# Kernel optimization log

Hardware: AMD Instinct MI355X
Metric: run time of the kernel (lower is better)

Reference implementation:

```python
import jax, jax.numpy as jnp
import numpy as np
from jax import lax

BN_EPS = 1e-5


def setup_inputs() -> dict:
    key = jax.random.key(0)
    ks = jax.random.split(key, 4)
    B, C1, H, W = 16, 256, 64, 64
    E, C2, K = 4, 256, 3
    x = jax.random.normal(ks[0], (B, C1, H, W), dtype=jnp.float32)
    w_route = jax.random.normal(ks[1], (E, C1), dtype=jnp.float32) * 0.02
    b_route = jnp.zeros((E,), dtype=jnp.float32)
    w_experts = jax.random.normal(ks[2], (E, C2, C1, K, K), dtype=jnp.float32) * 0.02
    bn_gamma = jnp.ones((C2,), dtype=jnp.float32)
    bn_beta = jnp.zeros((C2,), dtype=jnp.float32)
    bn_mean = jnp.zeros((C2,), dtype=jnp.float32)
    bn_var = jnp.ones((C2,), dtype=jnp.float32)
    return {"x": x, "w_route": w_route, "b_route": b_route,
            "w_experts": w_experts, "bn_gamma": bn_gamma, "bn_beta": bn_beta,
            "bn_mean": bn_mean, "bn_var": bn_var}


def reference(x, w_route, b_route, w_experts, bn_gamma, bn_beta, bn_mean, bn_var):
    # Routing: global average pool -> linear -> sigmoid. [B, E]
    pooled = jnp.mean(x, axis=(2, 3))
    routing = jax.nn.sigmoid(pooled @ w_route.T + b_route)

    # All num_experts conv passes in one grouped-output conv (same math as the
    # per-expert loop in the original): stack expert filters along out-channels.
    E, Co, Ci, kh, kw = w_experts.shape
    w = w_experts.reshape(E * Co, Ci, kh, kw)
    pad = kh // 2  # autopad(3) = 1
    y = lax.conv_general_dilated(
        x, w, window_strides=(1, 1), padding=[(pad, pad), (pad, pad)],
        dimension_numbers=("NCHW", "OIHW", "NCHW"))  # [B, E*Co, H, W]
    B, _, Ho, Wo = y.shape
    y = y.reshape(B, E, Co, Ho, Wo)

    # Per-sample weighted sum over experts.
    out = jnp.einsum("beohw,be->bohw", y, routing)

    # BatchNorm2d (inference form: running stats) + SiLU.
    inv = bn_gamma / jnp.sqrt(bn_var + BN_EPS)
    out = out * inv[None, :, None, None] + (bn_beta - bn_mean * inv)[None, :, None, None]
    return jax.nn.silu(out)
```

## Files before the change

kernel.cpp:

```cpp
#include <hip/hip_runtime.h>
#include <stdint.h>

typedef unsigned int uint;
typedef unsigned short ushort;
typedef __attribute__((ext_vector_type(8))) short short8;
typedef __attribute__((ext_vector_type(4))) float f32x4;

__device__ float  g_pooled[16 * 256];
__device__ ushort g_wct[16 * 9 * 256 * 256];
__device__ ushort g_xt[16 * 64 * 64 * 256];
__device__ uint   g_isf32;

__device__ __forceinline__ float bf2f(ushort u) {
    return __uint_as_float(((uint)u) << 16);
}
__device__ __forceinline__ ushort f2bf(float f) {
    uint u = __float_as_uint(f);
    return (ushort)((u + 0x7fffu + ((u >> 16) & 1u)) >> 16);
}

__global__ void detect_zero_kernel(const uint* __restrict__ bn_g_u) {
    int t = threadIdx.x;
    for (int i = t; i < 16 * 256; i += 256) g_pooled[i] = 0.f;
    if (t == 0) g_isf32 = (bn_g_u[0] == 0x3F800000u) ? 1u : 0u;
}

__global__ __launch_bounds__(256) void xt_pool_kernel(const void* __restrict__ xraw) {
    __shared__ float tf[64 * 65];
    uint* tile = (uint*)tf;
    const int c0 = blockIdx.x * 64, h = blockIdx.y, b = blockIdx.z;
    const int t = threadIdx.x;
    uint* xtu = (uint*)g_xt;
    const uint isf32 = g_isf32;
    if (isf32) {
        const float* xf = (const float*)xraw;
#pragma unroll
        for (int p = 0; p < 16; ++p) {
            int idx = p * 256 + t;
            int cil = idx >> 6, w = idx & 63;
            tf[cil * 65 + w] = xf[(((size_t)(b * 256 + c0 + cil)) * 64 + h) * 64 + w];
        }
        __syncthreads();
#pragma unroll
        for (int p = 0; p < 8; ++p) {
            int w = p * 8 + (t >> 5), cid = t & 31;
            uint lo = f2bf(tf[(2 * cid) * 65 + w]);
            uint hi = f2bf(tf[(2 * cid + 1) * 65 + w]);
            xtu[(((size_t)b * 64 + h) * 64 + w) * 128 + (c0 >> 1) + cid] = lo | (hi << 16);
        }
        if (t < 64) {
            float s = 0.f;
#pragma unroll
            for (int w = 0; w < 64; ++w) s += tf[t * 65 + w];
            atomicAdd(&g_pooled[b * 256 + c0 + t], s);
        }
    } else {
        const uint* xu = (const uint*)xraw;
#pragma unroll
        for (int p = 0; p < 8; ++p) {
            int cil = p * 8 + (t >> 5), wd = t & 31;
            tile[cil * 33 + wd] =
                xu[(((size_t)(b * 256 + c0 + cil)) * 64 + h) * 32 + wd];
        }
        __syncthreads();
#pragma unroll
        for (int p = 0; p < 8; ++p) {
            int w = p * 8 + (t >> 5), cid = t & 31;
            uint a = tile[(2 * cid) * 33 + (w >> 1)];
            uint bb = tile[(2 * cid + 1) * 33 + (w >> 1)];
            uint lo = (w & 1) ? (a >> 16) : (a & 0xffffu);
            uint hi = (w & 1) ? (bb >> 16) : (bb & 0xffffu);
            xtu[(((size_t)b * 64 + h) * 64 + w) * 128 + (c0 >> 1) + cid] = lo | (hi << 16);
        }
        if (t < 64) {
            float s = 0.f;
#pragma unroll
            for (int wd = 0; wd < 32; ++wd) {
                uint u = tile[t * 33 + wd];
                s += __uint_as_float(u << 16) + __uint_as_float(u & 0xffff0000u);
            }
            atomicAdd(&g_pooled[b * 256 + c0 + t], s);
        }
    }
}

__global__ __launch_bounds__(256) void wcomb_kernel(const void* __restrict__ w_exp,
                                                    const void* __restrict__ w_route,
                                                    const void* __restrict__ b_route) {
    __shared__ float s_rout[64];
    const int co = blockIdx.x, ci = threadIdx.x;
    const uint isf32 = g_isf32;
    if (ci < 64) {
        int b = ci >> 2, e = ci & 3;
        float s;
        if (isf32) {
            const float* wr = (const float*)w_route;
            s = ((const float*)b_route)[e];
            for (int c = 0; c < 256; ++c)
                s += g_pooled[b * 256 + c] * (1.f / 4096.f) * wr[e * 256 + c];
        } else {
            const ushort* wr = (const ushort*)w_route;
            s = bf2f(((const ushort*)b_route)[e]);
            for (int c = 0; c < 256; ++c)
                s += g_pooled[b * 256 + c] * (1.f / 4096.f) * bf2f(wr[e * 256 + c]);
        }
        s_rout[ci] = 1.f / (1.f + __expf(-s));
    }
    float we[4][9];
    if (isf32) {
        const float* wf = (const float*)w_exp;
#pragma unroll
        for (int e = 0; e < 4; ++e) {
            const float* p = wf + (((size_t)e * 256 + co) * 256 + ci) * 9;
#pragma unroll
            for (int tp = 0; tp < 9; ++tp) we[e][tp] = p[tp];
        }
    } else {
        const ushort* wb = (const ushort*)w_exp;
#pragma unroll
        for (int e = 0; e < 4; ++e) {
            const ushort* p = wb + (((size_t)e * 256 + co) * 256 + ci) * 9;
#pragma unroll
            for (int tp = 0; tp < 9; ++tp) we[e][tp] = bf2f(p[tp]);
        }
    }
    __syncthreads();
    for (int b = 0; b < 16; ++b) {
        float r0 = s_rout[b * 4 + 0], r1 = s_rout[b * 4 + 1];
        float r2 = s_rout[b * 4 + 2], r3 = s_rout[b * 4 + 3];
#pragma unroll
        for (int tp = 0; tp < 9; ++tp) {
            float a = r0 * we[0][tp] + r1 * we[1][tp] + r2 * we[2][tp] + r3 * we[3][tp];
            g_wct[(((size_t)b * 9 + tp) * 256 + co) * 256 + ci] = f2bf(a);
        }
    }
}

__device__ __forceinline__ void load_iter(int it, int t, int h0,
                                          const ushort* __restrict__ wct_p,
                                          const ushort* __restrict__ xt_p,
                                          short8 wv[6], short8 xv[2]) {
    const int cc = it / 3, kh = it - cc * 3;
    const int ci0 = cc * 32;
#pragma unroll
    for (int i = 0; i < 6; ++i) {
        int f = i * 4096 + t * 16;
        int kw = f >> 13;
        int rem = f & 8191;
        int col = rem >> 6;
        int cio = (rem & 63) >> 1;
        wv[i] = *(const short8*)(wct_p +
            (((size_t)(kh * 3 + kw) * 256 + col) * 256 + ci0 + cio));
    }
#pragma unroll
    for (int i = 0; i < 2; ++i) {
        int f = i * 4096 + t * 16;
        int r = f >> 12;
        int rem = f & 4095;
        int col = rem >> 6;
        int cio = (rem & 63) >> 1;
        int h_in = h0 + kh - 1 + r;
        if (h_in >= 0 && h_in < 64)
            xv[i] = *(const short8*)(xt_p + (((size_t)h_in * 64 + col) * 256 + ci0 + cio));
        else
            xv[i] = (short8){0, 0, 0, 0, 0, 0, 0, 0};
    }
}

__global__ __launch_bounds__(256) void conv_kernel(
    const void* __restrict__ bn_g, const void* __restrict__ bn_b,
    const void* __restrict__ bn_m, const void* __restrict__ bn_v,
    void* __restrict__ outv) {
    __shared__ __align__(16) ushort s_x[2 * 66 * 32];
    __shared__ __align__(16) ushort s_w[3 * 128 * 32];
    __shared__ float bn_inv[128], bn_add[128];

    const int t = threadIdx.x;
    const int lane = t & 63;
    const int q = lane >> 4, l16 = lane & 15;
    const int wave = __builtin_amdgcn_readfirstlane(t >> 6);
    const int u = blockIdx.x;
    const int pair = u & 31, hw = u >> 5;
    const int b = pair >> 1;
    const int co0 = (pair & 1) * 128;
    const int h0 = hw * 2;
    const int wm = wave & 1, wn = wave >> 1;
    const uint isf32 = g_isf32;

    if (t < 128) {
        int co = co0 + t;
        float g, be, mn, vr;
        if (isf32) {
            g = ((const float*)bn_g)[co]; be = ((const float*)bn_b)[co];
            mn = ((const float*)bn_m)[co]; vr = ((const float*)bn_v)[co];
        } else {
            g = bf2f(((const ushort*)bn_g)[co]); be = bf2f(((const ushort*)bn_b)[co]);
            mn = bf2f(((const ushort*)bn_m)[co]); vr = bf2f(((const ushort*)bn_v)[co]);
        }
        float inv = g * __frsqrt_rn(vr + 1e-5f);
        bn_inv[t] = inv;
        bn_add[t] = be - mn * inv;
        int r = t >> 6, side = (t >> 5) & 1, ci = t & 31;
        s_x[(r * 66 + side * 65) * 32 + ci] = 0;
    }

    f32x4 acc[4][4];
#pragma unroll
    for (int mt = 0; mt < 4; ++mt)
#pragma unroll
        for (int nt = 0; nt < 4; ++nt) acc[mt][nt] = (f32x4){0.f, 0.f, 0.f, 0.f};

    const ushort* xt_p  = g_xt  + (size_t)b * 64 * 64 * 256;
    const ushort* wct_p = g_wct + (size_t)b * 9 * 256 * 256 + (size_t)co0 * 256;

    short8 wv[6], xv[2];
    load_iter(0, t, h0, wct_p, xt_p, wv, xv);

    for (int it = 0; it < 24; ++it) {
        __syncthreads();
#pragma unroll
        for (int i = 0; i < 6; ++i)
            *(short8*)((char*)s_w + i * 4096 + t * 16) = wv[i];
#pragma unroll
        for (int i = 0; i < 2; ++i) {
            int f = i * 4096 + t * 16;
            int r = f >> 12;
            int rem = f & 4095;
            *(short8*)((char*)s_x + r * 4224 + 64 + rem) = xv[i];
        }
        __syncthreads();
        short8 wv2[6], xv2[2];
        int itn = (it + 1 < 24) ? it + 1 : 23;
        load_iter(itn, t, h0, wct_p, xt_p, wv2, xv2);
#pragma unroll
        for (int kw = 0; kw < 3; ++kw) {
            short8 a[4], bf[4];
#pragma unroll
            for (int mt = 0; mt < 4; ++mt)
                a[mt] = *(const short8*)(s_w + ((kw * 128 + wm * 64 + mt * 16 + l16) * 32 + q * 8));
#pragma unroll
            for (int nt = 0; nt < 4; ++nt)
                bf[nt] = *(const short8*)(s_x + ((wn * 66 + nt * 16 + l16 + kw) * 32 + q * 8));
#pragma unroll
            for (int mt = 0; mt < 4; ++mt)
#pragma unroll
                for (int nt = 0; nt < 4; ++nt)
                    acc[mt][nt] = __builtin_amdgcn_mfma_f32_16x16x32_bf16(
                        a[mt], bf[nt], acc[mt][nt], 0, 0, 0);
        }
#pragma unroll
        for (int i = 0; i < 6; ++i) wv[i] = wv2[i];
        xv[0] = xv2[0]; xv[1] = xv2[1];
    }

#pragma unroll
    for (int mt = 0; mt < 4; ++mt) {
        int co_l = wm * 64 + mt * 16 + q * 4;
#pragma unroll
        for (int i = 0; i < 4; ++i) {
            float inv = bn_inv[co_l + i], add = bn_add[co_l + i];
            int co = co0 + co_l + i;
#pragma unroll
            for (int nt = 0; nt < 4; ++nt) {
                int n_local = wn * 64 + nt * 16 + l16;
                int h = h0 + (n_local >> 6), w = n_local & 63;
                float v = acc[mt][nt][i] * inv + add;
                float s = v / (1.f + __expf(-v));
                size_t idx = (((size_t)b * 256 + co) * 64 + h) * 64 + w;
                if (isf32) ((float*)outv)[idx] = s;
                else       ((ushort*)outv)[idx] = f2bf(s);
            }
        }
    }
}

extern "C" void kernel_launch(void* const* d_in, const int* in_sizes, int n_in,
                              void* d_out, int out_size, void* d_ws, size_t ws_size,
                              hipStream_t stream) {
    const void* x       = d_in[0];
    const void* w_route = d_in[1];
    const void* b_route = d_in[2];
    const void* w_exp   = d_in[3];
    const void* bn_g    = d_in[4];
    const void* bn_b    = d_in[5];
    const void* bn_m    = d_in[6];
    const void* bn_v    = d_in[7];
    (void)d_ws; (void)ws_size;

    detect_zero_kernel<<<1, 256, 0, stream>>>((const uint*)bn_g);
    xt_pool_kernel<<<dim3(4, 64, 16), 256, 0, stream>>>(x);
    wcomb_kernel<<<256, 256, 0, stream>>>(w_exp, w_route, b_route);
    conv_kernel<<<1024, 256, 0, stream>>>(bn_g, bn_b, bn_m, bn_v, d_out);
}
```

Baseline: 256.4 us.

## Vectorize transpose and weight-combine loads, pad conv LDS rows against bank conflicts

The x transpose kernel now reads float4 and writes uint4 instead of scalar elements. The weight-combine kernel stages expert weights through shared memory with coalesced float4 loads and splits the routing dot products across all threads with a reduction. The conv kernel pads its LDS rows from 32 to 40 bf16 elements so the MFMA operand reads hit fewer LDS bank conflicts, at the cost of more shared memory per block.

Result: no change. 257.2 us (+0.3%).

```diff
diff --git a/kernel.cpp b/kernel.cpp
--- a/kernel.cpp
+++ b/kernel.cpp
@@ -33,20 +33,31 @@
     uint* xtu = (uint*)g_xt;
     const uint isf32 = g_isf32;
     if (isf32) {
-        const float* xf = (const float*)xraw;
-#pragma unroll
-        for (int p = 0; p < 16; ++p) {
+        const float4* xf4 = (const float4*)xraw;
+#pragma unroll
+        for (int p = 0; p < 4; ++p) {
             int idx = p * 256 + t;
-            int cil = idx >> 6, w = idx & 63;
-            tf[cil * 65 + w] = xf[(((size_t)(b * 256 + c0 + cil)) * 64 + h) * 64 + w];
-        }
-        __syncthreads();
-#pragma unroll
-        for (int p = 0; p < 8; ++p) {
-            int w = p * 8 + (t >> 5), cid = t & 31;
-            uint lo = f2bf(tf[(2 * cid) * 65 + w]);
-            uint hi = f2bf(tf[(2 * cid + 1) * 65 + w]);
-            xtu[(((size_t)b * 64 + h) * 64 + w) * 128 + (c0 >> 1) + cid] = lo | (hi << 16);
+            int cil = idx >> 4, w4 = idx & 15;
+            float4 v = xf4[((((size_t)(b * 256 + c0 + cil)) * 64 + h) * 64 >> 2) + w4];
+            tf[cil * 65 + w4 * 4 + 0] = v.x;
+            tf[cil * 65 + w4 * 4 + 1] = v.y;
+            tf[cil * 65 + w4 * 4 + 2] = v.z;
+            tf[cil * 65 + w4 * 4 + 3] = v.w;
+        }
+        __syncthreads();
+#pragma unroll
+        for (int p = 0; p < 2; ++p) {
+            int idx = p * 256 + t;
+            int w = idx >> 3, g = idx & 7;
+            uint4 o;
+            uint* op = (uint*)&o;
+#pragma unroll
+            for (int k = 0; k < 4; ++k) {
+                uint lo = f2bf(tf[(8 * g + 2 * k) * 65 + w]);
+                uint hi = f2bf(tf[(8 * g + 2 * k + 1) * 65 + w]);
+                op[k] = lo | (hi << 16);
+            }
+            ((uint4*)xtu)[(((((size_t)b * 64 + h) * 64 + w) * 128) + (c0 >> 1) + 4 * g) >> 2] = o;
         }
         if (t < 64) {
             float s = 0.f;
@@ -87,51 +98,67 @@
 __global__ __launch_bounds__(256) void wcomb_kernel(const void* __restrict__ w_exp,
                                                     const void* __restrict__ w_route,
                                                     const void* __restrict__ b_route) {
+    __shared__ float sw[4 * 2304];
+    __shared__ float red[256];
     __shared__ float s_rout[64];
-    const int co = blockIdx.x, ci = threadIdx.x;
+    const int co = blockIdx.x, t = threadIdx.x;
     const uint isf32 = g_isf32;
-    if (ci < 64) {
-        int b = ci >> 2, e = ci & 3;
-        float s;
-        if (isf32) {
+    float we[4][9];
+    if (isf32) {
+        const float4* wf4 = (const float4*)w_exp;
+#pragma unroll
+        for (int j = 0; j < 9; ++j) {
+            int idx = j * 256 + t;
+            int e = idx / 576, rem = idx - e * 576;
+            ((float4*)sw)[e * 576 + rem] =
+                wf4[(((size_t)e * 65536 + (size_t)co * 256) * 9 >> 2) + rem];
+        }
+        {
+            int p = t >> 2, s4 = t & 3;
+            int b = p >> 2, e = p & 3;
             const float* wr = (const float*)w_route;
-            s = ((const float*)b_route)[e];
-            for (int c = 0; c < 256; ++c)
-                s += g_pooled[b * 256 + c] * (1.f / 4096.f) * wr[e * 256 + c];
-        } else {
+            float s = 0.f;
+            for (int c = s4 * 64; c < s4 * 64 + 64; ++c)
+                s += g_pooled[b * 256 + c] * wr[e * 256 + c];
+            red[t] = s;
+        }
+        __syncthreads();
+        if (t < 64) {
+            int e = t & 3;
+            float s = (red[t * 4] + red[t * 4 + 1] + red[t * 4 + 2] + red[t * 4 + 3])
+                      * (1.f / 4096.f) + ((const float*)b_route)[e];
+            s_rout[t] = 1.f / (1.f + __expf(-s));
+        }
+        __syncthreads();
+#pragma unroll
+        for (int e = 0; e < 4; ++e)
+#pragma unroll
+            for (int tp = 0; tp < 9; ++tp) we[e][tp] = sw[e * 2304 + t * 9 + tp];
+    } else {
+        const ushort* wb = (const ushort*)w_exp;
+#pragma unroll
+        for (int e = 0; e < 4; ++e) {
+            const ushort* p = wb + (((size_t)e * 256 + co) * 256 + t) * 9;
+#pragma unroll
+            for (int tp = 0; tp < 9; ++tp) we[e][tp] = bf2f(p[tp]);
+        }
+        if (t < 64) {
+            int b = t >> 2, e = t & 3;
             const ushort* wr = (const ushort*)w_route;
-            s = bf2f(((const ushort*)b_route)[e]);
+            float s = bf2f(((const ushort*)b_route)[e]);
             for (int c = 0; c < 256; ++c)
                 s += g_pooled[b * 256 + c] * (1.f / 4096.f) * bf2f(wr[e * 256 + c]);
-        }
-        s_rout[ci] = 1.f / (1.f + __expf(-s));
-    }
-    float we[4][9];
-    if (isf32) {
-        const float* wf = (const float*)w_exp;
-#pragma unroll
-        for (int e = 0; e < 4; ++e) {
-            const float* p = wf + (((size_t)e * 256 + co) * 256 + ci) * 9;
-#pragma unroll
-            for (int tp = 0; tp < 9; ++tp) we[e][tp] = p[tp];
-        }
-    } else {
-        const ushort* wb = (const ushort*)w_exp;
-#pragma unroll
-        for (int e = 0; e < 4; ++e) {
-            const ushort* p = wb + (((size_t)e * 256 + co) * 256 + ci) * 9;
-#pragma unroll
-            for (int tp = 0; tp < 9; ++tp) we[e][tp] = bf2f(p[tp]);
-        }
-    }
-    __syncthreads();
+            s_rout[t] = 1.f / (1.f + __expf(-s));
+        }
+        __syncthreads();
+    }
     for (int b = 0; b < 16; ++b) {
         float r0 = s_rout[b * 4 + 0], r1 = s_rout[b * 4 + 1];
         float r2 = s_rout[b * 4 + 2], r3 = s_rout[b * 4 + 3];
 #pragma unroll
         for (int tp = 0; tp < 9; ++tp) {
             float a = r0 * we[0][tp] + r1 * we[1][tp] + r2 * we[2][tp] + r3 * we[3][tp];
-            g_wct[(((size_t)b * 9 + tp) * 256 + co) * 256 + ci] = f2bf(a);
+            g_wct[(((size_t)b * 9 + tp) * 256 + co) * 256 + t] = f2bf(a);
         }
     }
 }
@@ -171,8 +198,8 @@
     const void* __restrict__ bn_g, const void* __restrict__ bn_b,
     const void* __restrict__ bn_m, const void* __restrict__ bn_v,
     void* __restrict__ outv) {
-    __shared__ __align__(16) ushort s_x[2 * 66 * 32];
-    __shared__ __align__(16) ushort s_w[3 * 128 * 32];
+    __shared__ __align__(16) ushort s_x[132 * 40];
+    __shared__ __align__(16) ushort s_w[384 * 40];
     __shared__ float bn_inv[128], bn_add[128];
 
     const int t = threadIdx.x;
@@ -201,7 +228,7 @@
         bn_inv[t] = inv;
         bn_add[t] = be - mn * inv;
         int r = t >> 6, side = (t >> 5) & 1, ci = t & 31;
-        s_x[(r * 66 + side * 65) * 32 + ci] = 0;
+        s_x[(r * 66 + side * 65) * 40 + ci] = 0;
     }
 
     f32x4 acc[4][4];
@@ -219,14 +246,17 @@
     for (int it = 0; it < 24; ++it) {
         __syncthreads();
 #pragma unroll
-        for (int i = 0; i < 6; ++i)
-            *(short8*)((char*)s_w + i * 4096 + t * 16) = wv[i];
+        for (int i = 0; i < 6; ++i) {
+            int f = i * 4096 + t * 16;
+            *(short8*)((char*)s_w + (f >> 6) * 80 + (f & 63)) = wv[i];
+        }
 #pragma unroll
         for (int i = 0; i < 2; ++i) {
             int f = i * 4096 + t * 16;
             int r = f >> 12;
             int rem = f & 4095;
-            *(short8*)((char*)s_x + r * 4224 + 64 + rem) = xv[i];
+            int R = r * 66 + 1 + (rem >> 6);
+            *(short8*)((char*)s_x + R * 80 + (rem & 63)) = xv[i];
         }
         __syncthreads();
         short8 wv2[6], xv2[2];
@@ -237,10 +267,10 @@
             short8 a[4], bf[4];
 #pragma unroll
             for (int mt = 0; mt < 4; ++mt)
-                a[mt] = *(const short8*)(s_w + ((kw * 128 + wm * 64 + mt * 16 + l16) * 32 + q * 8));
+                a[mt] = *(const short8*)(s_w + (kw * 128 + wm * 64 + mt * 16 + l16) * 40 + q * 8);
 #pragma unroll
             for (int nt = 0; nt < 4; ++nt)
-                bf[nt] = *(const short8*)(s_x + ((wn * 66 + nt * 16 + l16 + kw) * 32 + q * 8));
+                bf[nt] = *(const short8*)(s_x + (wn * 66 + nt * 16 + l16 + kw) * 40 + q * 8);
 #pragma unroll
             for (int mt = 0; mt < 4; ++mt)
 #pragma unroll
```
